# Kernel tuning notes

Measured on AMD Instinct MI355X. Metric: run time of the kernel, lower is better.

The kernel has to match this reference:

```python
import jax, jax.numpy as jnp
import numpy as np

T, B, D = 1024, 4, 1024
E, K = 8, 2
H = int(round(2.0 * D))   # options.transformer_dim_scale = 2.0
O = D


def setup_inputs() -> dict:
    key = jax.random.key(0)
    ks = jax.random.split(key, 8)
    s = lambda fan: 1.0 / np.sqrt(fan)
    return {
        "x": jax.random.normal(ks[0], (T, B, D), dtype=jnp.float32),
        "sequence_mask": jnp.ones((T, B, 1), dtype=jnp.float32),
        "ln_scale": jnp.ones((D,), dtype=jnp.float32),
        "ln_bias": jnp.zeros((D,), dtype=jnp.float32),
        "router_w": jax.random.normal(ks[1], (E, D), dtype=jnp.float32) * s(D),
        "w1": jax.random.normal(ks[2], (E, D, H), dtype=jnp.float32) * s(D),
        "b1": jnp.zeros((E, H), dtype=jnp.float32),
        "w2": jax.random.normal(ks[3], (E, H, O), dtype=jnp.float32) * s(H),
        "b2": jnp.zeros((E, O), dtype=jnp.float32),
    }


def _layernorm(x, scale, bias, eps=1e-5):
    mu = jnp.mean(x, axis=-1, keepdims=True)
    var = jnp.mean(jnp.square(x - mu), axis=-1, keepdims=True)
    return (x - mu) * jax.lax.rsqrt(var + eps) * scale + bias


def reference(x, sequence_mask, ln_scale, ln_bias, router_w, w1, b1, w2, b2):
    t, b, d = x.shape
    n = t * b  # total tokens
    xn = _layernorm(x, ln_scale, ln_bias)
    x_flat = xn.reshape(n, d)                                  # [N, D]

    gate_logits = x_flat @ router_w.T                          # [N, E]
    topk_logits, topk_idx = jax.lax.top_k(gate_logits, K)      # [N, K]
    gate_probs = jax.nn.softmax(topk_logits, axis=-1)          # [N, K]
    # scatter top-k probs into a dense [N, E] combine-weight matrix
    rows = jnp.arange(n)[:, None]
    weights = jnp.zeros((n, E), dtype=x.dtype).at[rows, topk_idx].add(gate_probs)

    # dense per-expert two-layer MLP (exact GELU, dropout=0 at inference)
    h = jax.nn.gelu(jnp.einsum('nd,edh->neh', x_flat, w1) + b1, approximate=False)
    y = jax.nn.gelu(jnp.einsum('neh,eho->neo', h, w2) + b2, approximate=False)
    out = jnp.einsum('neo,ne->no', y, weights).reshape(t, b, O)

    out = out * sequence_mask                                  # multiplicative masking
    return out, gate_logits
```

## Files before the change

### kernel.cpp

```cpp
#include <hip/hip_runtime.h>
#include <hip/hip_bf16.h>
#include <math.h>

#define T_DIM 1024
#define B_DIM 4
#define D_DIM 1024
#define N_TOK (T_DIM * B_DIM)
#define E_NUM 8
#define K_TOP 2
#define H_DIM 2048
#define O_DIM 1024
#define MAX_YSLOTS 72

typedef __attribute__((ext_vector_type(8))) short bf16x8;
typedef __attribute__((ext_vector_type(4))) float f32x4;

__device__ __forceinline__ float gelu_exact(float x) {
    return 0.5f * x * (1.0f + erff(x * 0.7071067811865476f));
}

__device__ __forceinline__ unsigned short f2bf(float f) {
    union { __hip_bfloat16 h; unsigned short u; } c;
    c.h = __float2bfloat16(f);
    return c.u;
}

__device__ __forceinline__ void gload_lds16(const void* g, void* l) {
    __builtin_amdgcn_global_load_lds(
        (const __attribute__((address_space(1))) void*)g,
        (__attribute__((address_space(3))) void*)l,
        16, 0, 0);
}

__global__ __launch_bounds__(256) void ln_router_kernel(
    const float* __restrict__ x,
    const float* __restrict__ seq_mask,
    const float* __restrict__ ln_scale,
    const float* __restrict__ ln_bias,
    const float* __restrict__ router_w,
    unsigned short* __restrict__ xn,
    float* __restrict__ gate_out,
    unsigned int* __restrict__ tok_e,
    float2* __restrict__ tok_p)
{
    const int wv = threadIdx.x >> 6;
    const int ln = threadIdx.x & 63;
    const int n = blockIdx.x * 4 + wv;

    const float* xr = x + (size_t)n * D_DIM;

    float v[4][4];
    float sum = 0.f, sumsq = 0.f;
#pragma unroll
    for (int p = 0; p < 4; ++p) {
        float4 t = *(const float4*)&xr[ln * 4 + p * 256];
        v[p][0] = t.x; v[p][1] = t.y; v[p][2] = t.z; v[p][3] = t.w;
#pragma unroll
        for (int c = 0; c < 4; ++c) { sum += v[p][c]; sumsq += v[p][c] * v[p][c]; }
    }
#pragma unroll
    for (int m = 1; m < 64; m <<= 1) {
        sum   += __shfl_xor(sum, m, 64);
        sumsq += __shfl_xor(sumsq, m, 64);
    }
    const float mu = sum * (1.0f / D_DIM);
    const float var = sumsq * (1.0f / D_DIM) - mu * mu;
    const float rstd = rsqrtf(var + 1e-5f);

    float xv[4][4];
#pragma unroll
    for (int p = 0; p < 4; ++p) {
        int col = ln * 4 + p * 256;
        float4 sc = *(const float4*)&ln_scale[col];
        float4 bi = *(const float4*)&ln_bias[col];
        const float* scp = (const float*)&sc;
        const float* bip = (const float*)&bi;
        ushort4 o;
        unsigned short* op = (unsigned short*)&o;
#pragma unroll
        for (int c = 0; c < 4; ++c) {
            float t = (v[p][c] - mu) * rstd * scp[c] + bip[c];
            xv[p][c] = t;
            op[c] = f2bf(t);
        }
        *(ushort4*)&xn[(size_t)n * D_DIM + col] = o;
    }

    float dot[E_NUM];
#pragma unroll
    for (int e = 0; e < E_NUM; ++e) {
        const float* rw = router_w + (size_t)e * D_DIM;
        float a = 0.f;
#pragma unroll
        for (int p = 0; p < 4; ++p) {
            float4 t = *(const float4*)&rw[ln * 4 + p * 256];
            const float* tp = (const float*)&t;
#pragma unroll
            for (int c = 0; c < 4; ++c) a += xv[p][c] * tp[c];
        }
        dot[e] = a;
    }
#pragma unroll
    for (int e = 0; e < E_NUM; ++e)
#pragma unroll
        for (int m = 1; m < 64; m <<= 1) dot[e] += __shfl_xor(dot[e], m, 64);

    if (ln == 0) {
        float4 g0 = make_float4(dot[0], dot[1], dot[2], dot[3]);
        float4 g1 = make_float4(dot[4], dot[5], dot[6], dot[7]);
        *(float4*)&gate_out[(size_t)n * E_NUM] = g0;
        *(float4*)&gate_out[(size_t)n * E_NUM + 4] = g1;

        int i0 = 0; float l0 = dot[0];
        for (int e = 1; e < E_NUM; ++e)
            if (dot[e] > l0) { l0 = dot[e]; i0 = e; }
        int i1 = -1; float l1 = -INFINITY;
        for (int e = 0; e < E_NUM; ++e) {
            if (e == i0) continue;
            if (dot[e] > l1) { l1 = dot[e]; i1 = e; }
        }
        float z = __expf(l1 - l0);
        float p0 = 1.0f / (1.0f + z);
        float p1 = z / (1.0f + z);
        float msk = seq_mask[n];

        tok_e[n] = (unsigned)i0 | ((unsigned)i1 << 8);
        tok_p[n] = make_float2(p0 * msk, p1 * msk);
    }
}

__global__ __launch_bounds__(256) void build_lists(
    const unsigned int* __restrict__ tok_e,
    const float2* __restrict__ tok_p,
    int* __restrict__ counts,
    int* __restrict__ perm,
    int* __restrict__ hrow,
    float* __restrict__ probs)
{
    const int e = blockIdx.x;
    const int tid = threadIdx.x;
    const int wv = tid >> 6, ln = tid & 63;
    __shared__ int s_base;
    __shared__ int wave_tot[4];
    if (tid == 0) s_base = 0;
    __syncthreads();

    for (int t0 = 0; t0 < N_TOK; t0 += 256) {
        int t = t0 + tid;
        unsigned pk = tok_e[t];
        int m1 = (((pk >> 8) & 0xffu) == (unsigned)e);
        int m = (((pk & 0xffu) == (unsigned)e) | m1);
        unsigned long long bal = __ballot(m);
        int pre = __popcll(bal & ((1ull << ln) - 1ull));
        if (ln == 0) wave_tot[wv] = __popcll(bal);
        __syncthreads();
        int base = s_base;
        int wbase = 0;
#pragma unroll
        for (int w = 0; w < 4; ++w) if (w < wv) wbase += wave_tot[w];
        int total = wave_tot[0] + wave_tot[1] + wave_tot[2] + wave_tot[3];
        __syncthreads();
        if (m) {
            int pos = base + wbase + pre;
            perm[e * N_TOK + pos] = t;
            hrow[e * N_TOK + pos] = t * 2 + m1;
            float2 p = tok_p[t];
            probs[e * N_TOK + pos] = m1 ? p.y : p.x;
        }
        if (tid == 0) s_base = base + total;
        __syncthreads();
    }
    if (tid == 0) counts[e] = s_base;
}

__global__ __launch_bounds__(256) void transpose_convert(
    const float* __restrict__ src, unsigned short* __restrict__ dst,
    int K, int N)
{
    __shared__ float ts[64][65];
    const int e = blockIdx.z;
    const int n0 = blockIdx.x * 64;
    const int k0 = blockIdx.y * 64;
    const float* S = src + (size_t)e * K * N;
    unsigned short* D = dst + (size_t)e * N * K;
    const int tid = threadIdx.x;
    const int r = tid >> 4, c4 = (tid & 15) * 4;

#pragma unroll
    for (int j = 0; j < 4; ++j) {
        float4 v = *(const float4*)&S[(size_t)(k0 + r + 16 * j) * N + n0 + c4];
        ts[r + 16 * j][c4 + 0] = v.x;
        ts[r + 16 * j][c4 + 1] = v.y;
        ts[r + 16 * j][c4 + 2] = v.z;
        ts[r + 16 * j][c4 + 3] = v.w;
    }
    __syncthreads();
#pragma unroll
    for (int j = 0; j < 4; ++j) {
        int nn = r + 16 * j;
        ushort4 o;
        o.x = f2bf(ts[c4 + 0][nn]);
        o.y = f2bf(ts[c4 + 1][nn]);
        o.z = f2bf(ts[c4 + 2][nn]);
        o.w = f2bf(ts[c4 + 3][nn]);
        *(ushort4*)&D[(size_t)(n0 + nn) * K + k0 + c4] = o;
    }
}

__device__ __forceinline__ int slot_to_tile(const int* counts, int yslot, int* m0) {
    int e = -1, acc = 0, m = 0;
#pragma unroll
    for (int ee = 0; ee < E_NUM; ++ee) {
        int t = (counts[ee] + 127) >> 7;
        if (e < 0 && yslot < acc + t) { e = ee; m = (yslot - acc) << 7; }
        acc += t;
    }
    *m0 = m;
    return e;
}

__global__ __launch_bounds__(256) void expert_gemm1(
    const unsigned short* __restrict__ xn,
    const unsigned short* __restrict__ wt1,
    const float* __restrict__ b1,
    const int* __restrict__ counts,
    const int* __restrict__ perm,
    const int* __restrict__ hrow,
    unsigned short* __restrict__ hbuf)
{
    int m0;
    const int e = slot_to_tile(counts, blockIdx.y, &m0);
    if (e < 0) return;
    const int cnt = counts[e];
    const int n0 = blockIdx.x * 128;
    const int tid = threadIdx.x;
    const int wv = tid >> 6, ln = tid & 63;
    const int ml = ln & 15, q = ln >> 4;
    const int wm = (wv & 1) * 64, wn = (wv >> 1) * 64;

    __shared__ __align__(16) unsigned char As[128 * 64];
    __shared__ __align__(16) unsigned char Bs[128 * 64];
    __shared__ int s_tok[128];
    __shared__ int s_hr[128];

    if (tid < 128) {
        int m = m0 + tid;
        int ok = (m < cnt);
        s_tok[tid] = ok ? perm[e * N_TOK + m] : 0;
        s_hr[tid]  = ok ? hrow[e * N_TOK + m] : 0;
    }
    __syncthreads();

    const unsigned short* wte = wt1 + (size_t)e * H_DIM * D_DIM;
    const unsigned short* agp[2]; int alds[2];
    const unsigned short* bgp[2]; int blds[2];
#pragma unroll
    for (int j = 0; j < 2; ++j) {
        int slot = j * 256 + tid;
        int r = slot >> 2, ss = slot & 3;
        int sg = ss ^ ((r >> 1) & 3);
        agp[j] = xn + (size_t)s_tok[r] * D_DIM + sg * 8;
        alds[j] = slot * 16;
        bgp[j] = wte + (size_t)(n0 + r) * D_DIM + sg * 8;
        blds[j] = slot * 16;
    }

    f32x4 acc[4][4] = {};
    const int rslot = (q ^ ((ml >> 1) & 3)) * 16;

    for (int k0 = 0; k0 < D_DIM; k0 += 32) {
        __syncthreads();
#pragma unroll
        for (int j = 0; j < 2; ++j) {
            gload_lds16(agp[j] + k0, As + alds[j]);
            gload_lds16(bgp[j] + k0, Bs + blds[j]);
        }
        __syncthreads();
        bf16x8 af[4], bfr[4];
#pragma unroll
        for (int i = 0; i < 4; ++i)
            af[i] = *(const bf16x8*)(As + (wm + i * 16 + ml) * 64 + rslot);
#pragma unroll
        for (int j = 0; j < 4; ++j)
            bfr[j] = *(const bf16x8*)(Bs + (wn + j * 16 + ml) * 64 + rslot);
#pragma unroll
        for (int i = 0; i < 4; ++i)
#pragma unroll
            for (int j = 0; j < 4; ++j)
                acc[i][j] = __builtin_amdgcn_mfma_f32_16x16x32_bf16(
                    af[i], bfr[j], acc[i][j], 0, 0, 0);
    }

    float bias[4];
#pragma unroll
    for (int j = 0; j < 4; ++j)
        bias[j] = b1[(size_t)e * H_DIM + n0 + wn + j * 16 + ml];

#pragma unroll
    for (int i = 0; i < 4; ++i) {
#pragma unroll
        for (int r = 0; r < 4; ++r) {
            int rl = wm + i * 16 + q * 4 + r;
            if (m0 + rl < cnt) {
                int hr = s_hr[rl];
                unsigned short* dst = hbuf + (size_t)hr * H_DIM + n0 + wn + ml;
#pragma unroll
                for (int j = 0; j < 4; ++j)
                    dst[j * 16] = f2bf(gelu_exact(acc[i][j][r] + bias[j]));
            }
        }
    }
}

__global__ __launch_bounds__(512) void expert_gemm2(
    const unsigned short* __restrict__ hbuf,
    const unsigned short* __restrict__ wt2,
    const float* __restrict__ b2,
    const int* __restrict__ counts,
    const int* __restrict__ perm,
    const int* __restrict__ hrow,
    const float* __restrict__ probs,
    float* __restrict__ ybuf)
{
    int m0;
    const int e = slot_to_tile(counts, blockIdx.y, &m0);
    if (e < 0) return;
    const int cnt = counts[e];
    const int n0 = blockIdx.x * 128;
    const int tid = threadIdx.x;
    const int wv = tid >> 6, ln = tid & 63;
    const int ml = ln & 15, q = ln >> 4;
    const int wm = (wv & 3) * 32;
    const int wn = (wv >> 2) * 64;

    __shared__ __align__(16) unsigned char As[128 * 64];
    __shared__ __align__(16) unsigned char Bs[128 * 64];
    __shared__ int s_hr[128];
    __shared__ float s_p[128];

    if (tid < 128) {
        int m = m0 + tid;
        int ok = (m < cnt);
        s_hr[tid] = ok ? hrow[e * N_TOK + m] : 0;
        s_p[tid]  = ok ? probs[e * N_TOK + m] : 0.f;
    }
    __syncthreads();

    const unsigned short* wte = wt2 + (size_t)e * O_DIM * H_DIM;
    const int r_ = tid >> 2, ss = tid & 3;
    const int sg = ss ^ ((r_ >> 1) & 3);
    const unsigned short* agp = hbuf + (size_t)s_hr[r_] * H_DIM + sg * 8;
    const int alds = tid * 16;
    const unsigned short* bgp = wte + (size_t)(n0 + r_) * H_DIM + sg * 8;
    const int blds = tid * 16;

    f32x4 acc[2][4] = {};
    const int rslot = (q ^ ((ml >> 1) & 3)) * 16;

    for (int k0 = 0; k0 < H_DIM; k0 += 32) {
        __syncthreads();
        gload_lds16(agp + k0, As + alds);
        gload_lds16(bgp + k0, Bs + blds);
        __syncthreads();
        bf16x8 af[2], bfr[4];
#pragma unroll
        for (int i = 0; i < 2; ++i)
            af[i] = *(const bf16x8*)(As + (wm + i * 16 + ml) * 64 + rslot);
#pragma unroll
        for (int j = 0; j < 4; ++j)
            bfr[j] = *(const bf16x8*)(Bs + (wn + j * 16 + ml) * 64 + rslot);
#pragma unroll
        for (int i = 0; i < 2; ++i)
#pragma unroll
            for (int j = 0; j < 4; ++j)
                acc[i][j] = __builtin_amdgcn_mfma_f32_16x16x32_bf16(
                    af[i], bfr[j], acc[i][j], 0, 0, 0);
    }

    float bias[4];
#pragma unroll
    for (int j = 0; j < 4; ++j)
        bias[j] = b2[(size_t)e * O_DIM + n0 + wn + j * 16 + ml];

#pragma unroll
    for (int i = 0; i < 2; ++i) {
#pragma unroll
        for (int r = 0; r < 4; ++r) {
            int rl = wm + i * 16 + q * 4 + r;
            if (m0 + rl < cnt) {
                int hr = s_hr[rl];
                float p = s_p[rl];
                float* dst = ybuf + (size_t)hr * O_DIM + n0 + wn + ml;
#pragma unroll
                for (int j = 0; j < 4; ++j)
                    dst[j * 16] = gelu_exact(acc[i][j][r] + bias[j]) * p;
            }
        }
    }
}

__global__ __launch_bounds__(256) void combine_kernel(
    const float* __restrict__ ybuf, float* __restrict__ out)
{
    const size_t i = ((size_t)blockIdx.x * 256 + threadIdx.x) * 4;
    const size_t t = i / O_DIM;
    const size_t o = i % O_DIM;
    float4 a = *(const float4*)&ybuf[(t * 2) * O_DIM + o];
    float4 b = *(const float4*)&ybuf[(t * 2 + 1) * O_DIM + o];
    float4 r = make_float4(a.x + b.x, a.y + b.y, a.z + b.z, a.w + b.w);
    *(float4*)&out[i] = r;
}

extern "C" void kernel_launch(void* const* d_in, const int* in_sizes, int n_in,
                              void* d_out, int out_size, void* d_ws, size_t ws_size,
                              hipStream_t stream) {
    const float* x        = (const float*)d_in[0];
    const float* seq_mask = (const float*)d_in[1];
    const float* ln_scale = (const float*)d_in[2];
    const float* ln_bias  = (const float*)d_in[3];
    const float* router_w = (const float*)d_in[4];
    const float* w1       = (const float*)d_in[5];
    const float* b1       = (const float*)d_in[6];
    const float* w2       = (const float*)d_in[7];
    const float* b2       = (const float*)d_in[8];

    float* out      = (float*)d_out;
    float* gate_out = out + (size_t)N_TOK * O_DIM;

    char* ws = (char*)d_ws;
    unsigned short* xn = (unsigned short*)ws;
    ws += (size_t)N_TOK * D_DIM * 2;
    unsigned short* wt = (unsigned short*)ws;
    ws += (size_t)E_NUM * H_DIM * D_DIM * 2;
    unsigned short* hbuf = (unsigned short*)ws;
    ws += (size_t)N_TOK * K_TOP * H_DIM * 2;
    float* ybuf = (float*)ws;
    ws += (size_t)N_TOK * K_TOP * O_DIM * 4;
    unsigned int* tok_e = (unsigned int*)ws; ws += (size_t)N_TOK * 4;
    float2* tok_p = (float2*)ws; ws += (size_t)N_TOK * 8;
    int* counts = (int*)ws; ws += 256;
    int* perm = (int*)ws;  ws += (size_t)E_NUM * N_TOK * 4;
    int* hrow = (int*)ws;  ws += (size_t)E_NUM * N_TOK * 4;
    float* probs = (float*)ws;

    ln_router_kernel<<<N_TOK / 4, 256, 0, stream>>>(
        x, seq_mask, ln_scale, ln_bias, router_w,
        xn, gate_out, tok_e, tok_p);

    build_lists<<<E_NUM, 256, 0, stream>>>(
        tok_e, tok_p, counts, perm, hrow, probs);

    transpose_convert<<<dim3(H_DIM / 64, D_DIM / 64, E_NUM), 256, 0, stream>>>(
        w1, wt, D_DIM, H_DIM);

    expert_gemm1<<<dim3(H_DIM / 128, MAX_YSLOTS), 256, 0, stream>>>(
        xn, wt, b1, counts, perm, hrow, hbuf);

    transpose_convert<<<dim3(O_DIM / 64, H_DIM / 64, E_NUM), 256, 0, stream>>>(
        w2, wt, H_DIM, O_DIM);

    expert_gemm2<<<dim3(O_DIM / 128, MAX_YSLOTS), 512, 0, stream>>>(
        hbuf, wt, b2, counts, perm, hrow, probs, ybuf);

    combine_kernel<<<(N_TOK * O_DIM / 4) / 256, 256, 0, stream>>>(ybuf, out);
}
```

Before: 348.6 us.

## Double-buffer LDS tiles in both expert GEMM kernels

Both expert GEMM kernels now keep two LDS tile buffers. The loads for the next K-slice are issued right after a single barrier, and the MFMA work then runs on the current buffer. This replaces the old pattern of two barriers per iteration with serialized load-then-compute, so global-to-LDS traffic can overlap with matrix math. The cost is twice the LDS per block, which may lower occupancy, and correctness relies on the barrier draining the outstanding async loads.

```diff
diff --git a/kernel.cpp b/kernel.cpp
--- a/kernel.cpp
+++ b/kernel.cpp
@@ -219,6 +219,8 @@
     return e;
 }
 
+#define TBUF (128 * 64)
+
 __global__ __launch_bounds__(256) void expert_gemm1(
     const unsigned short* __restrict__ xn,
     const unsigned short* __restrict__ wt1,
@@ -238,8 +240,8 @@
     const int ml = ln & 15, q = ln >> 4;
     const int wm = (wv & 1) * 64, wn = (wv >> 1) * 64;
 
-    __shared__ __align__(16) unsigned char As[128 * 64];
-    __shared__ __align__(16) unsigned char Bs[128 * 64];
+    __shared__ __align__(16) unsigned char As[2 * TBUF];
+    __shared__ __align__(16) unsigned char Bs[2 * TBUF];
     __shared__ int s_tok[128];
     __shared__ int s_hr[128];
 
@@ -265,30 +267,42 @@
         blds[j] = slot * 16;
     }
 
+#pragma unroll
+    for (int j = 0; j < 2; ++j) {
+        gload_lds16(agp[j], As + alds[j]);
+        gload_lds16(bgp[j], Bs + blds[j]);
+    }
+
     f32x4 acc[4][4] = {};
     const int rslot = (q ^ ((ml >> 1) & 3)) * 16;
+    int cur = 0;
 
     for (int k0 = 0; k0 < D_DIM; k0 += 32) {
         __syncthreads();
-#pragma unroll
-        for (int j = 0; j < 2; ++j) {
-            gload_lds16(agp[j] + k0, As + alds[j]);
-            gload_lds16(bgp[j] + k0, Bs + blds[j]);
-        }
-        __syncthreads();
+        if (k0 + 32 < D_DIM) {
+            const int nb = (cur ^ 1) * TBUF;
+#pragma unroll
+            for (int j = 0; j < 2; ++j) {
+                gload_lds16(agp[j] + k0 + 32, As + nb + alds[j]);
+                gload_lds16(bgp[j] + k0 + 32, Bs + nb + blds[j]);
+            }
+        }
+        const unsigned char* Ab = As + cur * TBUF;
+        const unsigned char* Bb = Bs + cur * TBUF;
         bf16x8 af[4], bfr[4];
 #pragma unroll
         for (int i = 0; i < 4; ++i)
-            af[i] = *(const bf16x8*)(As + (wm + i * 16 + ml) * 64 + rslot);
+            af[i] = *(const bf16x8*)(Ab + (wm + i * 16 + ml) * 64 + rslot);
 #pragma unroll
         for (int j = 0; j < 4; ++j)
-            bfr[j] = *(const bf16x8*)(Bs + (wn + j * 16 + ml) * 64 + rslot);
+            bfr[j] = *(const bf16x8*)(Bb + (wn + j * 16 + ml) * 64 + rslot);
 #pragma unroll
         for (int i = 0; i < 4; ++i)
 #pragma unroll
             for (int j = 0; j < 4; ++j)
                 acc[i][j] = __builtin_amdgcn_mfma_f32_16x16x32_bf16(
                     af[i], bfr[j], acc[i][j], 0, 0, 0);
+        cur ^= 1;
     }
 
     float bias[4];
@@ -333,8 +347,8 @@
     const int wm = (wv & 3) * 32;
     const int wn = (wv >> 2) * 64;
 
-    __shared__ __align__(16) unsigned char As[128 * 64];
-    __shared__ __align__(16) unsigned char Bs[128 * 64];
+    __shared__ __align__(16) unsigned char As[2 * TBUF];
+    __shared__ __align__(16) unsigned char Bs[2 * TBUF];
     __shared__ int s_hr[128];
     __shared__ float s_p[128];
 
@@ -354,27 +368,36 @@
     const unsigned short* bgp = wte + (size_t)(n0 + r_) * H_DIM + sg * 8;
     const int blds = tid * 16;
 
+    gload_lds16(agp, As + alds);
+    gload_lds16(bgp, Bs + blds);
+
     f32x4 acc[2][4] = {};
     const int rslot = (q ^ ((ml >> 1) & 3)) * 16;
+    int cur = 0;
 
     for (int k0 = 0; k0 < H_DIM; k0 += 32) {
         __syncthreads();
-        gload_lds16(agp + k0, As + alds);
-        gload_lds16(bgp + k0, Bs + blds);
-        __syncthreads();
+        if (k0 + 32 < H_DIM) {
+            const int nb = (cur ^ 1) * TBUF;
+            gload_lds16(agp + k0 + 32, As + nb + alds);
+            gload_lds16(bgp + k0 + 32, Bs + nb + blds);
+        }
+        const unsigned char* Ab = As + cur * TBUF;
+        const unsigned char* Bb = Bs + cur * TBUF;
         bf16x8 af[2], bfr[4];
 #pragma unroll
         for (int i = 0; i < 2; ++i)
-            af[i] = *(const bf16x8*)(As + (wm + i * 16 + ml) * 64 + rslot);
+            af[i] = *(const bf16x8*)(Ab + (wm + i * 16 + ml) * 64 + rslot);
 #pragma unroll
         for (int j = 0; j < 4; ++j)
-            bfr[j] = *(const bf16x8*)(Bs + (wn + j * 16 + ml) * 64 + rslot);
+            bfr[j] = *(const bf16x8*)(Bb + (wn + j * 16 + ml) * 64 + rslot);
 #pragma unroll
         for (int i = 0; i < 2; ++i)
 #pragma unroll
             for (int j = 0; j < 4; ++j)
                 acc[i][j] = __builtin_amdgcn_mfma_f32_16x16x32_bf16(
                     af[i], bfr[j], acc[i][j], 0, 0, 0);
+        cur ^= 1;
     }
 
     float bias[4];
```

Result: no change. 352.2 us (+1.1%).

## Shrink expert GEMM N-tiles to 64 and store expert outputs in bf16

Applied to the files above, without the earlier changes.

Both expert GEMMs now use 128x64 tiles with 256 threads and a minimum-occupancy launch bound. This doubles the grid, so more of the 256 CUs have work for the roughly 64 active M-tiles, and it lowers register and LDS use per block. The per-slot expert outputs (ybuf) are now written as bf16 instead of fp32, and the combine kernel reads them back as bf16. This halves that intermediate's memory traffic, at the cost of extra rounding before the final sum and reloading each A tile for twice as many N blocks.

```diff
diff --git a/kernel.cpp b/kernel.cpp
--- a/kernel.cpp
+++ b/kernel.cpp
@@ -23,6 +23,12 @@
     union { __hip_bfloat16 h; unsigned short u; } c;
     c.h = __float2bfloat16(f);
     return c.u;
+}
+
+__device__ __forceinline__ float bf2f(unsigned short u) {
+    union { unsigned int i; float f; } c;
+    c.i = ((unsigned int)u) << 16;
+    return c.f;
 }
 
 __device__ __forceinline__ void gload_lds16(const void* g, void* l) {
@@ -219,7 +225,7 @@
     return e;
 }
 
-__global__ __launch_bounds__(256) void expert_gemm1(
+__global__ __launch_bounds__(256, 8) void expert_gemm1(
     const unsigned short* __restrict__ xn,
     const unsigned short* __restrict__ wt1,
     const float* __restrict__ b1,
@@ -232,14 +238,15 @@
     const int e = slot_to_tile(counts, blockIdx.y, &m0);
     if (e < 0) return;
     const int cnt = counts[e];
-    const int n0 = blockIdx.x * 128;
+    const int n0 = blockIdx.x * 64;
     const int tid = threadIdx.x;
     const int wv = tid >> 6, ln = tid & 63;
     const int ml = ln & 15, q = ln >> 4;
-    const int wm = (wv & 1) * 64, wn = (wv >> 1) * 64;
+    const int wm = (wv & 1) * 64;
+    const int wn = (wv >> 1) * 32;
 
     __shared__ __align__(16) unsigned char As[128 * 64];
-    __shared__ __align__(16) unsigned char Bs[128 * 64];
+    __shared__ __align__(16) unsigned char Bs[64 * 64];
     __shared__ int s_tok[128];
     __shared__ int s_hr[128];
 
@@ -253,7 +260,6 @@
 
     const unsigned short* wte = wt1 + (size_t)e * H_DIM * D_DIM;
     const unsigned short* agp[2]; int alds[2];
-    const unsigned short* bgp[2]; int blds[2];
 #pragma unroll
     for (int j = 0; j < 2; ++j) {
         int slot = j * 256 + tid;
@@ -261,39 +267,39 @@
         int sg = ss ^ ((r >> 1) & 3);
         agp[j] = xn + (size_t)s_tok[r] * D_DIM + sg * 8;
         alds[j] = slot * 16;
-        bgp[j] = wte + (size_t)(n0 + r) * D_DIM + sg * 8;
-        blds[j] = slot * 16;
-    }
-
-    f32x4 acc[4][4] = {};
+    }
+    const int rb = tid >> 2, ssb = tid & 3;
+    const int sgb = ssb ^ ((rb >> 1) & 3);
+    const unsigned short* bgp = wte + (size_t)(n0 + rb) * D_DIM + sgb * 8;
+    const int blds = tid * 16;
+
+    f32x4 acc[4][2] = {};
     const int rslot = (q ^ ((ml >> 1) & 3)) * 16;
 
     for (int k0 = 0; k0 < D_DIM; k0 += 32) {
         __syncthreads();
-#pragma unroll
-        for (int j = 0; j < 2; ++j) {
-            gload_lds16(agp[j] + k0, As + alds[j]);
-            gload_lds16(bgp[j] + k0, Bs + blds[j]);
-        }
-        __syncthreads();
-        bf16x8 af[4], bfr[4];
+        gload_lds16(agp[0] + k0, As + alds[0]);
+        gload_lds16(agp[1] + k0, As + alds[1]);
+        gload_lds16(bgp + k0, Bs + blds);
+        __syncthreads();
+        bf16x8 af[4], bfr[2];
 #pragma unroll
         for (int i = 0; i < 4; ++i)
             af[i] = *(const bf16x8*)(As + (wm + i * 16 + ml) * 64 + rslot);
 #pragma unroll
-        for (int j = 0; j < 4; ++j)
+        for (int j = 0; j < 2; ++j)
             bfr[j] = *(const bf16x8*)(Bs + (wn + j * 16 + ml) * 64 + rslot);
 #pragma unroll
         for (int i = 0; i < 4; ++i)
 #pragma unroll
-            for (int j = 0; j < 4; ++j)
+            for (int j = 0; j < 2; ++j)
                 acc[i][j] = __builtin_amdgcn_mfma_f32_16x16x32_bf16(
                     af[i], bfr[j], acc[i][j], 0, 0, 0);
     }
 
-    float bias[4];
-#pragma unroll
-    for (int j = 0; j < 4; ++j)
+    float bias[2];
+#pragma unroll
+    for (int j = 0; j < 2; ++j)
         bias[j] = b1[(size_t)e * H_DIM + n0 + wn + j * 16 + ml];
 
 #pragma unroll
@@ -305,14 +311,14 @@
                 int hr = s_hr[rl];
                 unsigned short* dst = hbuf + (size_t)hr * H_DIM + n0 + wn + ml;
 #pragma unroll
-                for (int j = 0; j < 4; ++j)
+                for (int j = 0; j < 2; ++j)
                     dst[j * 16] = f2bf(gelu_exact(acc[i][j][r] + bias[j]));
             }
         }
     }
 }
 
-__global__ __launch_bounds__(512) void expert_gemm2(
+__global__ __launch_bounds__(256, 8) void expert_gemm2(
     const unsigned short* __restrict__ hbuf,
     const unsigned short* __restrict__ wt2,
     const float* __restrict__ b2,
@@ -320,21 +326,21 @@
     const int* __restrict__ perm,
     const int* __restrict__ hrow,
     const float* __restrict__ probs,
-    float* __restrict__ ybuf)
+    unsigned short* __restrict__ ybuf)
 {
     int m0;
     const int e = slot_to_tile(counts, blockIdx.y, &m0);
     if (e < 0) return;
     const int cnt = counts[e];
-    const int n0 = blockIdx.x * 128;
+    const int n0 = blockIdx.x * 64;
     const int tid = threadIdx.x;
     const int wv = tid >> 6, ln = tid & 63;
     const int ml = ln & 15, q = ln >> 4;
-    const int wm = (wv & 3) * 32;
-    const int wn = (wv >> 2) * 64;
+    const int wm = (wv & 1) * 64;
+    const int wn = (wv >> 1) * 32;
 
     __shared__ __align__(16) unsigned char As[128 * 64];
-    __shared__ __align__(16) unsigned char Bs[128 * 64];
+    __shared__ __align__(16) unsigned char Bs[64 * 64];
     __shared__ int s_hr[128];
     __shared__ float s_p[128];
 
@@ -347,67 +353,76 @@
     __syncthreads();
 
     const unsigned short* wte = wt2 + (size_t)e * O_DIM * H_DIM;
-    const int r_ = tid >> 2, ss = tid & 3;
-    const int sg = ss ^ ((r_ >> 1) & 3);
-    const unsigned short* agp = hbuf + (size_t)s_hr[r_] * H_DIM + sg * 8;
-    const int alds = tid * 16;
-    const unsigned short* bgp = wte + (size_t)(n0 + r_) * H_DIM + sg * 8;
+    const unsigned short* agp[2]; int alds[2];
+#pragma unroll
+    for (int j = 0; j < 2; ++j) {
+        int slot = j * 256 + tid;
+        int r = slot >> 2, ss = slot & 3;
+        int sg = ss ^ ((r >> 1) & 3);
+        agp[j] = hbuf + (size_t)s_hr[r] * H_DIM + sg * 8;
+        alds[j] = slot * 16;
+    }
+    const int rb = tid >> 2, ssb = tid & 3;
+    const int sgb = ssb ^ ((rb >> 1) & 3);
+    const unsigned short* bgp = wte + (size_t)(n0 + rb) * H_DIM + sgb * 8;
     const int blds = tid * 16;
 
-    f32x4 acc[2][4] = {};
+    f32x4 acc[4][2] = {};
     const int rslot = (q ^ ((ml >> 1) & 3)) * 16;
 
     for (int k0 = 0; k0 < H_DIM; k0 += 32) {
         __syncthreads();
-        gload_lds16(agp + k0, As + alds);
+        gload_lds16(agp[0] + k0, As + alds[0]);
+        gload_lds16(agp[1] + k0, As + alds[1]);
         gload_lds16(bgp + k0, Bs + blds);
         __syncthreads();
-        bf16x8 af[2], bfr[4];
-#pragma unroll
-        for (int i = 0; i < 2; ++i)
+        bf16x8 af[4], bfr[2];
+#pragma unroll
+        for (int i = 0; i < 4; ++i)
             af[i] = *(const bf16x8*)(As + (wm + i * 16 + ml) * 64 + rslot);
 #pragma unroll
-        for (int j = 0; j < 4; ++j)
+        for (int j = 0; j < 2; ++j)
             bfr[j] = *(const bf16x8*)(Bs + (wn + j * 16 + ml) * 64 + rslot);
 #pragma unroll
-        for (int i = 0; i < 2; ++i)
-#pragma unroll
-            for (int j = 0; j < 4; ++j)
+        for (int i = 0; i < 4; ++i)
+#pragma unroll
+            for (int j = 0; j < 2; ++j)
                 acc[i][j] = __builtin_amdgcn_mfma_f32_16x16x32_bf16(
                     af[i], bfr[j], acc[i][j], 0, 0, 0);
     }
 
-    float bias[4];
-#pragma unroll
-    for (int j = 0; j < 4; ++j)
+    float bias[2];
+#pragma unroll
+    for (int j = 0; j < 2; ++j)
         bias[j] = b2[(size_t)e * O_DIM + n0 + wn + j * 16 + ml];
 
 #pragma unroll
-    for (int i = 0; i < 2; ++i) {
+    for (int i = 0; i < 4; ++i) {
 #pragma unroll
         for (int r = 0; r < 4; ++r) {
             int rl = wm + i * 16 + q * 4 + r;
             if (m0 + rl < cnt) {
                 int hr = s_hr[rl];
                 float p = s_p[rl];
-                float* dst = ybuf + (size_t)hr * O_DIM + n0 + wn + ml;
-#pragma unroll
-                for (int j = 0; j < 4; ++j)
-                    dst[j * 16] = gelu_exact(acc[i][j][r] + bias[j]) * p;
+                unsigned short* dst = ybuf + (size_t)hr * O_DIM + n0 + wn + ml;
+#pragma unroll
+                for (int j = 0; j < 2; ++j)
+                    dst[j * 16] = f2bf(gelu_exact(acc[i][j][r] + bias[j]) * p);
             }
         }
     }
 }
 
 __global__ __launch_bounds__(256) void combine_kernel(
-    const float* __restrict__ ybuf, float* __restrict__ out)
+    const unsigned short* __restrict__ ybuf, float* __restrict__ out)
 {
     const size_t i = ((size_t)blockIdx.x * 256 + threadIdx.x) * 4;
     const size_t t = i / O_DIM;
     const size_t o = i % O_DIM;
-    float4 a = *(const float4*)&ybuf[(t * 2) * O_DIM + o];
-    float4 b = *(const float4*)&ybuf[(t * 2 + 1) * O_DIM + o];
-    float4 r = make_float4(a.x + b.x, a.y + b.y, a.z + b.z, a.w + b.w);
+    ushort4 a = *(const ushort4*)&ybuf[(t * 2) * O_DIM + o];
+    ushort4 b = *(const ushort4*)&ybuf[(t * 2 + 1) * O_DIM + o];
+    float4 r = make_float4(bf2f(a.x) + bf2f(b.x), bf2f(a.y) + bf2f(b.y),
+                           bf2f(a.z) + bf2f(b.z), bf2f(a.w) + bf2f(b.w));
     *(float4*)&out[i] = r;
 }
 
@@ -434,8 +449,8 @@
     ws += (size_t)E_NUM * H_DIM * D_DIM * 2;
     unsigned short* hbuf = (unsigned short*)ws;
     ws += (size_t)N_TOK * K_TOP * H_DIM * 2;
-    float* ybuf = (float*)ws;
-    ws += (size_t)N_TOK * K_TOP * O_DIM * 4;
+    unsigned short* ybuf = (unsigned short*)ws;
+    ws += (size_t)N_TOK * K_TOP * O_DIM * 2;
     unsigned int* tok_e = (unsigned int*)ws; ws += (size_t)N_TOK * 4;
     float2* tok_p = (float2*)ws; ws += (size_t)N_TOK * 8;
     int* counts = (int*)ws; ws += 256;
@@ -453,13 +468,13 @@
     transpose_convert<<<dim3(H_DIM / 64, D_DIM / 64, E_NUM), 256, 0, stream>>>(
         w1, wt, D_DIM, H_DIM);
 
-    expert_gemm1<<<dim3(H_DIM / 128, MAX_YSLOTS), 256, 0, stream>>>(
+    expert_gemm1<<<dim3(H_DIM / 64, MAX_YSLOTS), 256, 0, stream>>>(
         xn, wt, b1, counts, perm, hrow, hbuf);
 
     transpose_convert<<<dim3(O_DIM / 64, H_DIM / 64, E_NUM), 256, 0, stream>>>(
         w2, wt, H_DIM, O_DIM);
 
-    expert_gemm2<<<dim3(O_DIM / 128, MAX_YSLOTS), 512, 0, stream>>>(
+    expert_gemm2<<<dim3(O_DIM / 64, MAX_YSLOTS), 256, 0, stream>>>(
         hbuf, wt, b2, counts, perm, hrow, probs, ybuf);
 
     combine_kernel<<<(N_TOK * O_DIM / 4) / 256, 256, 0, stream>>>(ybuf, out);
```

Measured after the change: 377.9 us. 1.08x slower.
